# Performance work log

Hardware: AMD Instinct MI355X
Metric: run time of the kernel (lower is better)

## Reference

```python
import jax, jax.numpy as jnp
import numpy as np

N_NODES = 200000
N_EDGES = 6400000
IN_CH = 256
HID = 16


def gcn_conv(h, src, dst, deg_inv_sqrt, W, b, n_nodes):
    """One GCNConv (PyG semantics: add self-loops, symmetric norm, linear, scatter-add, bias)."""
    hw = h @ W  # [N, out]
    norm = deg_inv_sqrt[src] * deg_inv_sqrt[dst]  # [E]
    agg = jax.ops.segment_sum(norm[:, None] * hw[src], dst, num_segments=n_nodes)
    # self-loop contribution: deg_inv_sqrt[i]^2 * hw[i]
    agg = agg + hw * (deg_inv_sqrt ** 2)[:, None]
    return agg + b


def setup_inputs() -> dict:
    key = jax.random.key(0)
    k_x, k_e, k_w1, k_w2, k_w3 = jax.random.split(key, 5)
    x = jax.random.normal(k_x, (N_NODES, IN_CH), dtype=jnp.float32)
    edge_index = jax.random.randint(k_e, (2, N_EDGES), 0, N_NODES, dtype=jnp.int64)
    # Glorot-ish init for the three GCNConv weights, zeros for biases (PyG default)
    W1 = jax.random.normal(k_w1, (IN_CH, HID), dtype=jnp.float32) * (1.0 / np.sqrt(IN_CH))
    b1 = jnp.zeros((HID,), dtype=jnp.float32)
    W2 = jax.random.normal(k_w2, (HID, HID), dtype=jnp.float32) * (1.0 / np.sqrt(HID))
    b2 = jnp.zeros((HID,), dtype=jnp.float32)
    W3 = jax.random.normal(k_w3, (HID, 1), dtype=jnp.float32) * (1.0 / np.sqrt(HID))
    b3 = jnp.zeros((1,), dtype=jnp.float32)
    return {"x": x, "edge_index": edge_index, "W1": W1, "b1": b1,
            "W2": W2, "b2": b2, "W3": W3, "b3": b3}


def reference(x, edge_index, W1, b1, W2, b2, W3, b3):
    n_nodes = x.shape[0]
    src, dst = edge_index[0], edge_index[1]
    # GCN norm with self-loops: deg counts incoming edges + 1 self-loop
    deg = jax.ops.segment_sum(jnp.ones_like(dst, dtype=x.dtype), dst,
                              num_segments=n_nodes) + 1.0
    deg_inv_sqrt = deg ** -0.5  # deg >= 1, safe
    h = jax.nn.relu(gcn_conv(x, src, dst, deg_inv_sqrt, W1, b1, n_nodes))
    # dropout is identity in eval mode
    h = jax.nn.relu(gcn_conv(h, src, dst, deg_inv_sqrt, W2, b2, n_nodes))
    out = gcn_conv(h, src, dst, deg_inv_sqrt, W3, b3, n_nodes)  # [N, 1]
    return out
```

## Files before the change

### kernel.cpp

```cpp
#include <hip/hip_runtime.h>

#define NN 200000
#define EE 6400000L
#define NCB 196
#define CAP 36864
#define TILE 8192
#define NTILE 782

__device__ inline void f4add(float4& a, const float4 v) {
    a.x += v.x; a.y += v.y; a.z += v.z; a.w += v.w;
}

__global__ void k_detect(const int* __restrict__ w, int* __restrict__ flag,
                         int* __restrict__ gcur) {
    __shared__ int any;
    if (threadIdx.x == 0) any = 0;
    __syncthreads();
    int found = 0;
    for (int i = threadIdx.x; i < 8192; i += 256)
        if (w[2 * i + 1] != 0) found = 1;
    if (found) atomicOr(&any, 1);
    if (threadIdx.x < NCB) gcur[threadIdx.x] = threadIdx.x * CAP;
    __syncthreads();
    if (threadIdx.x == 0) flag[0] = any ? 0 : 1;
}

__global__ __launch_bounds__(256) void k_passA(
    const int* __restrict__ ew, const int* __restrict__ flag,
    int* __restrict__ gcur, unsigned* __restrict__ stage, long e) {
    __shared__ unsigned lv[TILE];
    __shared__ unsigned char lb[TILE];
    __shared__ int lh[NCB], lseg[NCB], lcur[NCB];
    for (int i = threadIdx.x; i < NCB; i += 256) { lh[i] = 0; lcur[i] = 0; }
    __syncthreads();
    long t0 = (long)blockIdx.x * TILE;
    int cnt = (int)min((long)TILE, e - t0);
    int shift = *flag;
    for (int i = threadIdx.x; i < cnt; i += 256) {
        int s = ew[(t0 + i) << shift];
        int d = ew[(EE + t0 + i) << shift];
        int b = d >> 10;
        lv[i] = (unsigned)s | ((unsigned)(d & 1023) << 18);
        lb[i] = (unsigned char)b;
        atomicAdd(&lh[b], 1);
    }
    __syncthreads();
    for (int i = threadIdx.x; i < NCB; i += 256)
        if (lh[i]) lseg[i] = atomicAdd(&gcur[i], lh[i]);
    __syncthreads();
    for (int i = threadIdx.x; i < cnt; i += 256) {
        int b = lb[i];
        int r = atomicAdd(&lcur[b], 1);
        stage[lseg[b] + r] = lv[i];
    }
}

__global__ __launch_bounds__(1024) void k_sortB(
    const unsigned* __restrict__ stage, const int* __restrict__ gcur,
    float* __restrict__ dis, int2* __restrict__ odn,
    unsigned* __restrict__ csr, int n) {
    __shared__ int cnt[1024];
    __shared__ int cur[1024];
    __shared__ int wsum[16];
    int t = threadIdx.x, B = blockIdx.x;
    cnt[t] = 0;
    __syncthreads();
    int s0 = B * CAP, s1 = gcur[B];
    for (int i = s0 + t; i < s1; i += 1024)
        atomicAdd(&cnt[stage[i] >> 18], 1);
    __syncthreads();
    int c = cnt[t];
    int pc = (c + 3) & ~3;
    int lane = t & 63, w = t >> 6;
    int s = pc;
#pragma unroll
    for (int o = 1; o < 64; o <<= 1) {
        int u = __shfl_up(s, o, 64);
        if (lane >= o) s += u;
    }
    if (lane == 63) wsum[w] = s;
    __syncthreads();
    int add = 0;
    for (int k = 0; k < w; ++k) add += wsum[k];
    int excl = s - pc + add;
    cur[t] = excl;
    int node = B * 1024 + t;
    if (node < n) {
        odn[node] = make_int2(s0 + excl, c);
        dis[node] = rsqrtf((float)(c + 1));
    }
    __syncthreads();
    for (int i = s0 + t; i < s1; i += 1024) {
        unsigned v = stage[i];
        int pos = s0 + atomicAdd(&cur[v >> 18], 1);
        csr[pos] = v & 0x3FFFF;
    }
}

__global__ __launch_bounds__(256) void k_mm1(
    const float* __restrict__ x, const float* __restrict__ W,
    const float* __restrict__ dis, float4* __restrict__ outr, int n) {
    __shared__ float Wl[256 * 16];
    int t = threadIdx.x;
#pragma unroll
    for (int i = 0; i < 4; ++i)
        ((float4*)Wl)[t + i * 256] = ((const float4*)W)[t + i * 256];
    __syncthreads();

    int node = blockIdx.x * 256 + t;
    if (node >= n) return;

    const float4* xr = (const float4*)(x + (long)node * 256);
    float acc[16];
#pragma unroll
    for (int o = 0; o < 16; ++o) acc[o] = 0.f;

#pragma unroll 8
    for (int kk = 0; kk < 64; ++kk) {
        float4 xv = xr[kk];
#pragma unroll
        for (int q = 0; q < 4; ++q) {
            float xs = (q == 0) ? xv.x : (q == 1) ? xv.y : (q == 2) ? xv.z : xv.w;
            const float4* wr = (const float4*)&Wl[(kk * 4 + q) * 16];
#pragma unroll
            for (int oo = 0; oo < 4; ++oo) {
                float4 wv = wr[oo];
                acc[oo * 4 + 0] = fmaf(xs, wv.x, acc[oo * 4 + 0]);
                acc[oo * 4 + 1] = fmaf(xs, wv.y, acc[oo * 4 + 1]);
                acc[oo * 4 + 2] = fmaf(xs, wv.z, acc[oo * 4 + 2]);
                acc[oo * 4 + 3] = fmaf(xs, wv.w, acc[oo * 4 + 3]);
            }
        }
    }
    float dv = dis[node];
#pragma unroll
    for (int q = 0; q < 4; ++q)
        outr[node * 4 + q] = make_float4(acc[q * 4] * dv, acc[q * 4 + 1] * dv,
                                         acc[q * 4 + 2] * dv, acc[q * 4 + 3] * dv);
}

__global__ __launch_bounds__(256) void k_mm2(
    const float4* __restrict__ hr, const float* __restrict__ W,
    const float* __restrict__ dis, float4* __restrict__ outr, int n) {
    __shared__ float Wl[256];
    if (threadIdx.x < 64) ((float4*)Wl)[threadIdx.x] = ((const float4*)W)[threadIdx.x];
    __syncthreads();
    int node = blockIdx.x * 256 + threadIdx.x;
    if (node >= n) return;
    float hv[16];
#pragma unroll
    for (int i = 0; i < 4; ++i) {
        float4 v = hr[node * 4 + i];
        hv[i * 4 + 0] = v.x; hv[i * 4 + 1] = v.y; hv[i * 4 + 2] = v.z; hv[i * 4 + 3] = v.w;
    }
    float acc[16];
#pragma unroll
    for (int o = 0; o < 16; ++o) acc[o] = 0.f;
#pragma unroll
    for (int k = 0; k < 16; ++k) {
        float xs = hv[k];
#pragma unroll
        for (int o = 0; o < 16; ++o) acc[o] = fmaf(xs, Wl[k * 16 + o], acc[o]);
    }
    float dv = dis[node];
#pragma unroll
    for (int q = 0; q < 4; ++q)
        outr[node * 4 + q] = make_float4(acc[q * 4] * dv, acc[q * 4 + 1] * dv,
                                         acc[q * 4 + 2] * dv, acc[q * 4 + 3] * dv);
}

__global__ __launch_bounds__(256) void k_mm3(
    const float4* __restrict__ hr, const float* __restrict__ W,
    const float* __restrict__ dis, float* __restrict__ hws3, int n) {
    int node = blockIdx.x * 256 + threadIdx.x;
    if (node >= n) return;
    float acc = 0.f;
#pragma unroll
    for (int i = 0; i < 4; ++i) {
        float4 v = hr[node * 4 + i];
        acc = fmaf(v.x, W[i * 4 + 0], acc);
        acc = fmaf(v.y, W[i * 4 + 1], acc);
        acc = fmaf(v.z, W[i * 4 + 2], acc);
        acc = fmaf(v.w, W[i * 4 + 3], acc);
    }
    hws3[node] = acc * dis[node];
}

template <int RELU>
__global__ __launch_bounds__(256) void k_g16(
    const int2* __restrict__ odn, const unsigned* __restrict__ csr,
    const float* __restrict__ dis, const float4* __restrict__ tab,
    const float* __restrict__ b, float4* __restrict__ outr, int n) {
    int t = threadIdx.x;
    int node = blockIdx.x * 64 + (t >> 2);
    int j = t & 3;
    if (node >= n) return;
    int2 od = odn[node];
    int s0 = od.x, dg = od.y;
    float4 aA = make_float4(0.f, 0.f, 0.f, 0.f);
    float4 aB = make_float4(0.f, 0.f, 0.f, 0.f);
    int k = 0;
    for (; k + 8 <= dg; k += 8) {
        uint4 eL = *(const uint4*)(csr + s0 + k);
        uint4 eH = *(const uint4*)(csr + s0 + k + 4);
        f4add(aA, tab[eL.x * 4 + j]);
        f4add(aB, tab[eH.x * 4 + j]);
        f4add(aA, tab[eL.y * 4 + j]);
        f4add(aB, tab[eH.y * 4 + j]);
        f4add(aA, tab[eL.z * 4 + j]);
        f4add(aB, tab[eH.z * 4 + j]);
        f4add(aA, tab[eL.w * 4 + j]);
        f4add(aB, tab[eH.w * 4 + j]);
    }
    if (k + 4 <= dg) {
        uint4 e = *(const uint4*)(csr + s0 + k);
        f4add(aA, tab[e.x * 4 + j]);
        f4add(aB, tab[e.y * 4 + j]);
        f4add(aA, tab[e.z * 4 + j]);
        f4add(aB, tab[e.w * 4 + j]);
        k += 4;
    }
    for (; k < dg; ++k)
        f4add(aA, tab[csr[s0 + k] * 4 + j]);
    f4add(aA, aB);
    f4add(aA, tab[node * 4 + j]);
    float dv = dis[node];
    float4 bb = ((const float4*)b)[j];
    float4 r = make_float4(fmaf(dv, aA.x, bb.x), fmaf(dv, aA.y, bb.y),
                           fmaf(dv, aA.z, bb.z), fmaf(dv, aA.w, bb.w));
    if (RELU) {
        r.x = fmaxf(r.x, 0.f); r.y = fmaxf(r.y, 0.f);
        r.z = fmaxf(r.z, 0.f); r.w = fmaxf(r.w, 0.f);
    }
    outr[node * 4 + j] = r;
}

__global__ __launch_bounds__(256) void k_g1(
    const int2* __restrict__ odn, const unsigned* __restrict__ csr,
    const float* __restrict__ dis, const float* __restrict__ hws3,
    const float* __restrict__ b, float* __restrict__ out, int n) {
    int t = threadIdx.x;
    int node = blockIdx.x * 16 + (t >> 4);
    int ln = t & 15;
    if (node >= n) return;
    int2 od = odn[node];
    int s0 = od.x, dg = od.y;
    float acc = 0.f;
    for (int k = ln; k < dg; k += 16)
        acc += hws3[csr[s0 + k]];
#pragma unroll
    for (int o = 8; o >= 1; o >>= 1) acc += __shfl_down(acc, o, 16);
    if (ln == 0)
        out[node] = fmaf(dis[node], acc + hws3[node], b[0]);
}

extern "C" void kernel_launch(void* const* d_in, const int* in_sizes, int n_in,
                              void* d_out, int out_size, void* d_ws, size_t ws_size,
                              hipStream_t stream) {
    const float* x  = (const float*)d_in[0];
    const int*   ew = (const int*)d_in[1];
    const float* W1 = (const float*)d_in[2];
    const float* b1 = (const float*)d_in[3];
    const float* W2 = (const float*)d_in[4];
    const float* b2 = (const float*)d_in[5];
    const float* W3 = (const float*)d_in[6];
    const float* b3 = (const float*)d_in[7];
    float* out = (float*)d_out;

    unsigned* stage = (unsigned*)d_ws;
    unsigned* csr   = stage + (long)NCB * CAP;
    int*      gcur  = (int*)(csr + (long)NCB * CAP);
    int*      flag  = gcur + 256;
    int2*     odn   = (int2*)(flag + 16);
    float*    dis   = (float*)(odn + 200704);
    float4*   bufA  = (float4*)(dis + 200704);
    float4*   bufB  = bufA + 4 * 200064;

    const int n = NN;
    const long e = EE;
    int nb = (n + 255) / 256;
    int gb = (n + 63) / 64;
    int g1b = (n + 15) / 16;

    k_detect<<<1, 256, 0, stream>>>(ew, flag, gcur);
    k_passA<<<NTILE, 256, 0, stream>>>(ew, flag, gcur, stage, e);
    k_sortB<<<NCB, 1024, 0, stream>>>(stage, gcur, dis, odn, csr, n);

    k_mm1<<<nb, 256, 0, stream>>>(x, W1, dis, bufA, n);
    k_g16<1><<<gb, 256, 0, stream>>>(odn, csr, dis, bufA, b1, bufB, n);
    k_mm2<<<nb, 256, 0, stream>>>(bufB, W2, dis, bufA, n);
    k_g16<1><<<gb, 256, 0, stream>>>(odn, csr, dis, bufA, b2, bufB, n);
    k_mm3<<<nb, 256, 0, stream>>>(bufB, W3, dis, (float*)bufA, n);
    k_g1<<<g1b, 256, 0, stream>>>(odn, csr, dis, (const float*)bufA, b3, out, n);
}
```

Baseline: 454.0 us.

## Overlap layer-1 matmul with edge binning and fuse small matmuls into gathers

Runs the x@W1 matmul in the same grid as the edge-binning pass using alternating block roles, and applies the degree scaling to hw1 inside the CSR sort kernel. The 16x16 and 16x1 matmuls are fused into the aggregation kernels, with shared-memory staging and a quad shuffle reduction. This removes three launches and the intermediate feature round trips, and lets the bandwidth-heavy x read overlap with the atomic-heavy binning. It also drops the bounds checks by relying on the node count dividing evenly by the block sizes.

```diff
diff --git a/kernel.cpp b/kernel.cpp
--- a/kernel.cpp
+++ b/kernel.cpp
@@ -11,6 +11,15 @@
     a.x += v.x; a.y += v.y; a.z += v.z; a.w += v.w;
 }
 
+union SMem {
+    struct {
+        unsigned lv[TILE];
+        unsigned char lb[TILE];
+        int lh[NCB], lseg[NCB], lcur[NCB];
+    } p;
+    float wl[256 * 16];
+};
+
 __global__ void k_detect(const int* __restrict__ w, int* __restrict__ flag,
                          int* __restrict__ gcur) {
     __shared__ int any;
@@ -25,40 +34,78 @@
     if (threadIdx.x == 0) flag[0] = any ? 0 : 1;
 }
 
-__global__ __launch_bounds__(256) void k_passA(
+__global__ __launch_bounds__(256) void k_fused(
     const int* __restrict__ ew, const int* __restrict__ flag,
-    int* __restrict__ gcur, unsigned* __restrict__ stage, long e) {
-    __shared__ unsigned lv[TILE];
-    __shared__ unsigned char lb[TILE];
-    __shared__ int lh[NCB], lseg[NCB], lcur[NCB];
-    for (int i = threadIdx.x; i < NCB; i += 256) { lh[i] = 0; lcur[i] = 0; }
-    __syncthreads();
-    long t0 = (long)blockIdx.x * TILE;
-    int cnt = (int)min((long)TILE, e - t0);
-    int shift = *flag;
-    for (int i = threadIdx.x; i < cnt; i += 256) {
-        int s = ew[(t0 + i) << shift];
-        int d = ew[(EE + t0 + i) << shift];
-        int b = d >> 10;
-        lv[i] = (unsigned)s | ((unsigned)(d & 1023) << 18);
-        lb[i] = (unsigned char)b;
-        atomicAdd(&lh[b], 1);
-    }
-    __syncthreads();
-    for (int i = threadIdx.x; i < NCB; i += 256)
-        if (lh[i]) lseg[i] = atomicAdd(&gcur[i], lh[i]);
-    __syncthreads();
-    for (int i = threadIdx.x; i < cnt; i += 256) {
-        int b = lb[i];
-        int r = atomicAdd(&lcur[b], 1);
-        stage[lseg[b] + r] = lv[i];
+    int* __restrict__ gcur, unsigned* __restrict__ stage,
+    const float* __restrict__ x, const float* __restrict__ W1,
+    float4* __restrict__ hw1, long e, int n) {
+    __shared__ SMem sm;
+    int t = threadIdx.x;
+    int role = blockIdx.x & 1;
+    int idx = blockIdx.x >> 1;
+
+    if (role == 0) {
+        for (int i = t; i < NCB; i += 256) { sm.p.lh[i] = 0; sm.p.lcur[i] = 0; }
+        __syncthreads();
+        long t0 = (long)idx * TILE;
+        int cnt = (int)min((long)TILE, e - t0);
+        int shift = *flag;
+        for (int i = t; i < cnt; i += 256) {
+            int s = ew[(t0 + i) << shift];
+            int d = ew[(EE + t0 + i) << shift];
+            int b = d >> 10;
+            sm.p.lv[i] = (unsigned)s | ((unsigned)(d & 1023) << 18);
+            sm.p.lb[i] = (unsigned char)b;
+            atomicAdd(&sm.p.lh[b], 1);
+        }
+        __syncthreads();
+        for (int i = t; i < NCB; i += 256)
+            if (sm.p.lh[i]) sm.p.lseg[i] = atomicAdd(&gcur[i], sm.p.lh[i]);
+        __syncthreads();
+        for (int i = t; i < cnt; i += 256) {
+            int b = sm.p.lb[i];
+            int r = atomicAdd(&sm.p.lcur[b], 1);
+            stage[sm.p.lseg[b] + r] = sm.p.lv[i];
+        }
+    } else {
+#pragma unroll
+        for (int i = 0; i < 4; ++i)
+            ((float4*)sm.wl)[t + i * 256] = ((const float4*)W1)[t + i * 256];
+        __syncthreads();
+        int node = idx * 256 + t;
+        if (node >= n) return;
+        const float4* xr = (const float4*)(x + (long)node * 256);
+        float acc[16];
+#pragma unroll
+        for (int o = 0; o < 16; ++o) acc[o] = 0.f;
+#pragma unroll 8
+        for (int kk = 0; kk < 64; ++kk) {
+            float4 xv = xr[kk];
+#pragma unroll
+            for (int q = 0; q < 4; ++q) {
+                float xs = (q == 0) ? xv.x : (q == 1) ? xv.y : (q == 2) ? xv.z : xv.w;
+                const float4* wr = (const float4*)&sm.wl[(kk * 4 + q) * 16];
+#pragma unroll
+                for (int oo = 0; oo < 4; ++oo) {
+                    float4 wv = wr[oo];
+                    acc[oo * 4 + 0] = fmaf(xs, wv.x, acc[oo * 4 + 0]);
+                    acc[oo * 4 + 1] = fmaf(xs, wv.y, acc[oo * 4 + 1]);
+                    acc[oo * 4 + 2] = fmaf(xs, wv.z, acc[oo * 4 + 2]);
+                    acc[oo * 4 + 3] = fmaf(xs, wv.w, acc[oo * 4 + 3]);
+                }
+            }
+        }
+#pragma unroll
+        for (int q = 0; q < 4; ++q)
+            hw1[(long)node * 4 + q] = make_float4(acc[q * 4], acc[q * 4 + 1],
+                                                  acc[q * 4 + 2], acc[q * 4 + 3]);
     }
 }
 
 __global__ __launch_bounds__(1024) void k_sortB(
     const unsigned* __restrict__ stage, const int* __restrict__ gcur,
     float* __restrict__ dis, int2* __restrict__ odn,
-    unsigned* __restrict__ csr, int n) {
+    unsigned* __restrict__ csr, float4* __restrict__ hw1, int n) {
     __shared__ int cnt[1024];
     __shared__ int cur[1024];
     __shared__ int wsum[16];
@@ -86,8 +133,15 @@
     cur[t] = excl;
     int node = B * 1024 + t;
     if (node < n) {
+        float dv = rsqrtf((float)(c + 1));
         odn[node] = make_int2(s0 + excl, c);
-        dis[node] = rsqrtf((float)(c + 1));
+        dis[node] = dv;
+        float4* row = hw1 + (long)node * 4;
+#pragma unroll
+        for (int q = 0; q < 4; ++q) {
+            float4 v = row[q];
+            row[q] = make_float4(v.x * dv, v.y * dv, v.z * dv, v.w * dv);
+        }
     }
     __syncthreads();
     for (int i = s0 + t; i < s1; i += 1024) {
@@ -97,104 +151,17 @@
     }
 }
 
-__global__ __launch_bounds__(256) void k_mm1(
-    const float* __restrict__ x, const float* __restrict__ W,
-    const float* __restrict__ dis, float4* __restrict__ outr, int n) {
-    __shared__ float Wl[256 * 16];
-    int t = threadIdx.x;
-#pragma unroll
-    for (int i = 0; i < 4; ++i)
-        ((float4*)Wl)[t + i * 256] = ((const float4*)W)[t + i * 256];
-    __syncthreads();
-
-    int node = blockIdx.x * 256 + t;
-    if (node >= n) return;
-
-    const float4* xr = (const float4*)(x + (long)node * 256);
-    float acc[16];
-#pragma unroll
-    for (int o = 0; o < 16; ++o) acc[o] = 0.f;
-
-#pragma unroll 8
-    for (int kk = 0; kk < 64; ++kk) {
-        float4 xv = xr[kk];
-#pragma unroll
-        for (int q = 0; q < 4; ++q) {
-            float xs = (q == 0) ? xv.x : (q == 1) ? xv.y : (q == 2) ? xv.z : xv.w;
-            const float4* wr = (const float4*)&Wl[(kk * 4 + q) * 16];
-#pragma unroll
-            for (int oo = 0; oo < 4; ++oo) {
-                float4 wv = wr[oo];
-                acc[oo * 4 + 0] = fmaf(xs, wv.x, acc[oo * 4 + 0]);
-                acc[oo * 4 + 1] = fmaf(xs, wv.y, acc[oo * 4 + 1]);
-                acc[oo * 4 + 2] = fmaf(xs, wv.z, acc[oo * 4 + 2]);
-                acc[oo * 4 + 3] = fmaf(xs, wv.w, acc[oo * 4 + 3]);
-            }
-        }
-    }
-    float dv = dis[node];
-#pragma unroll
-    for (int q = 0; q < 4; ++q)
-        outr[node * 4 + q] = make_float4(acc[q * 4] * dv, acc[q * 4 + 1] * dv,
-                                         acc[q * 4 + 2] * dv, acc[q * 4 + 3] * dv);
-}
-
-__global__ __launch_bounds__(256) void k_mm2(
-    const float4* __restrict__ hr, const float* __restrict__ W,
-    const float* __restrict__ dis, float4* __restrict__ outr, int n) {
-    __shared__ float Wl[256];
-    if (threadIdx.x < 64) ((float4*)Wl)[threadIdx.x] = ((const float4*)W)[threadIdx.x];
-    __syncthreads();
-    int node = blockIdx.x * 256 + threadIdx.x;
-    if (node >= n) return;
-    float hv[16];
-#pragma unroll
-    for (int i = 0; i < 4; ++i) {
-        float4 v = hr[node * 4 + i];
-        hv[i * 4 + 0] = v.x; hv[i * 4 + 1] = v.y; hv[i * 4 + 2] = v.z; hv[i * 4 + 3] = v.w;
-    }
-    float acc[16];
-#pragma unroll
-    for (int o = 0; o < 16; ++o) acc[o] = 0.f;
-#pragma unroll
-    for (int k = 0; k < 16; ++k) {
-        float xs = hv[k];
-#pragma unroll
-        for (int o = 0; o < 16; ++o) acc[o] = fmaf(xs, Wl[k * 16 + o], acc[o]);
-    }
-    float dv = dis[node];
-#pragma unroll
-    for (int q = 0; q < 4; ++q)
-        outr[node * 4 + q] = make_float4(acc[q * 4] * dv, acc[q * 4 + 1] * dv,
-                                         acc[q * 4 + 2] * dv, acc[q * 4 + 3] * dv);
-}
-
-__global__ __launch_bounds__(256) void k_mm3(
-    const float4* __restrict__ hr, const float* __restrict__ W,
-    const float* __restrict__ dis, float* __restrict__ hws3, int n) {
-    int node = blockIdx.x * 256 + threadIdx.x;
-    if (node >= n) return;
-    float acc = 0.f;
-#pragma unroll
-    for (int i = 0; i < 4; ++i) {
-        float4 v = hr[node * 4 + i];
-        acc = fmaf(v.x, W[i * 4 + 0], acc);
-        acc = fmaf(v.y, W[i * 4 + 1], acc);
-        acc = fmaf(v.z, W[i * 4 + 2], acc);
-        acc = fmaf(v.w, W[i * 4 + 3], acc);
-    }
-    hws3[node] = acc * dis[node];
-}
-
-template <int RELU>
-__global__ __launch_bounds__(256) void k_g16(
+__global__ __launch_bounds__(256) void k_g16a(
     const int2* __restrict__ odn, const unsigned* __restrict__ csr,
     const float* __restrict__ dis, const float4* __restrict__ tab,
-    const float* __restrict__ b, float4* __restrict__ outr, int n) {
+    const float* __restrict__ b1v, const float* __restrict__ W2,
+    float4* __restrict__ out2) {
+    __shared__ float h1s[64 * 17];
+    __shared__ float W2l[256];
     int t = threadIdx.x;
+    if (t < 64) ((float4*)W2l)[t] = ((const float4*)W2)[t];
     int node = blockIdx.x * 64 + (t >> 2);
     int j = t & 3;
-    if (node >= n) return;
     int2 od = odn[node];
     int s0 = od.x, dg = od.y;
     float4 aA = make_float4(0.f, 0.f, 0.f, 0.f);
@@ -225,14 +192,79 @@
     f4add(aA, aB);
     f4add(aA, tab[node * 4 + j]);
     float dv = dis[node];
-    float4 bb = ((const float4*)b)[j];
+    float4 bb = ((const float4*)b1v)[j];
     float4 r = make_float4(fmaf(dv, aA.x, bb.x), fmaf(dv, aA.y, bb.y),
                            fmaf(dv, aA.z, bb.z), fmaf(dv, aA.w, bb.w));
-    if (RELU) {
-        r.x = fmaxf(r.x, 0.f); r.y = fmaxf(r.y, 0.f);
-        r.z = fmaxf(r.z, 0.f); r.w = fmaxf(r.w, 0.f);
-    }
-    outr[node * 4 + j] = r;
+    r.x = fmaxf(r.x, 0.f); r.y = fmaxf(r.y, 0.f);
+    r.z = fmaxf(r.z, 0.f); r.w = fmaxf(r.w, 0.f);
+    int nl = t >> 2;
+    h1s[nl * 17 + 4 * j + 0] = r.x;
+    h1s[nl * 17 + 4 * j + 1] = r.y;
+    h1s[nl * 17 + 4 * j + 2] = r.z;
+    h1s[nl * 17 + 4 * j + 3] = r.w;
+    __syncthreads();
+    float4 acc = make_float4(0.f, 0.f, 0.f, 0.f);
+#pragma unroll
+    for (int kk = 0; kk < 16; ++kk) {
+        float hv = h1s[nl * 17 + kk];
+        float4 wv = ((const float4*)&W2l[kk * 16])[j];
+        acc.x = fmaf(hv, wv.x, acc.x);
+        acc.y = fmaf(hv, wv.y, acc.y);
+        acc.z = fmaf(hv, wv.z, acc.z);
+        acc.w = fmaf(hv, wv.w, acc.w);
+    }
+    out2[(long)node * 4 + j] = make_float4(acc.x * dv, acc.y * dv,
+                                           acc.z * dv, acc.w * dv);
+}
+
+__global__ __launch_bounds__(256) void k_g16b(
+    const int2* __restrict__ odn, const unsigned* __restrict__ csr,
+    const float* __restrict__ dis, const float4* __restrict__ tab,
+    const float* __restrict__ b2v, const float* __restrict__ W3,
+    float* __restrict__ hws3) {
+    int t = threadIdx.x;
+    int node = blockIdx.x * 64 + (t >> 2);
+    int j = t & 3;
+    int2 od = odn[node];
+    int s0 = od.x, dg = od.y;
+    float4 aA = make_float4(0.f, 0.f, 0.f, 0.f);
+    float4 aB = make_float4(0.f, 0.f, 0.f, 0.f);
+    int k = 0;
+    for (; k + 8 <= dg; k += 8) {
+        uint4 eL = *(const uint4*)(csr + s0 + k);
+        uint4 eH = *(const uint4*)(csr + s0 + k + 4);
+        f4add(aA, tab[eL.x * 4 + j]);
+        f4add(aB, tab[eH.x * 4 + j]);
+        f4add(aA, tab[eL.y * 4 + j]);
+        f4add(aB, tab[eH.y * 4 + j]);
+        f4add(aA, tab[eL.z * 4 + j]);
+        f4add(aB, tab[eH.z * 4 + j]);
+        f4add(aA, tab[eL.w * 4 + j]);
+        f4add(aB, tab[eH.w * 4 + j]);
+    }
+    if (k + 4 <= dg) {
+        uint4 e = *(const uint4*)(csr + s0 + k);
+        f4add(aA, tab[e.x * 4 + j]);
+        f4add(aB, tab[e.y * 4 + j]);
+        f4add(aA, tab[e.z * 4 + j]);
+        f4add(aB, tab[e.w * 4 + j]);
+        k += 4;
+    }
+    for (; k < dg; ++k)
+        f4add(aA, tab[csr[s0 + k] * 4 + j]);
+    f4add(aA, aB);
+    f4add(aA, tab[node * 4 + j]);
+    float dv = dis[node];
+    float4 bb = ((const float4*)b2v)[j];
+    float4 r = make_float4(fmaf(dv, aA.x, bb.x), fmaf(dv, aA.y, bb.y),
+                           fmaf(dv, aA.z, bb.z), fmaf(dv, aA.w, bb.w));
+    r.x = fmaxf(r.x, 0.f); r.y = fmaxf(r.y, 0.f);
+    r.z = fmaxf(r.z, 0.f); r.w = fmaxf(r.w, 0.f);
+    float4 w3 = ((const float4*)W3)[j];
+    float pd = r.x * w3.x + r.y * w3.y + r.z * w3.z + r.w * w3.w;
+    pd += __shfl_xor(pd, 1, 4);
+    pd += __shfl_xor(pd, 2, 4);
+    if (j == 0) hws3[node] = pd * dv;
 }
 
 __global__ __launch_bounds__(256) void k_g1(
@@ -278,18 +310,13 @@
 
     const int n = NN;
     const long e = EE;
-    int nb = (n + 255) / 256;
-    int gb = (n + 63) / 64;
-    int g1b = (n + 15) / 16;
+    int gb = n / 64;
+    int g1b = n / 16;
 
     k_detect<<<1, 256, 0, stream>>>(ew, flag, gcur);
-    k_passA<<<NTILE, 256, 0, stream>>>(ew, flag, gcur, stage, e);
-    k_sortB<<<NCB, 1024, 0, stream>>>(stage, gcur, dis, odn, csr, n);
-
-    k_mm1<<<nb, 256, 0, stream>>>(x, W1, dis, bufA, n);
-    k_g16<1><<<gb, 256, 0, stream>>>(odn, csr, dis, bufA, b1, bufB, n);
-    k_mm2<<<nb, 256, 0, stream>>>(bufB, W2, dis, bufA, n);
-    k_g16<1><<<gb, 256, 0, stream>>>(odn, csr, dis, bufA, b2, bufB, n);
-    k_mm3<<<nb, 256, 0, stream>>>(bufB, W3, dis, (float*)bufA, n);
+    k_fused<<<2 * NTILE, 256, 0, stream>>>(ew, flag, gcur, stage, x, W1, bufA, e, n);
+    k_sortB<<<NCB, 1024, 0, stream>>>(stage, gcur, dis, odn, csr, bufA, n);
+    k_g16a<<<gb, 256, 0, stream>>>(odn, csr, dis, bufA, b1, W2, bufB);
+    k_g16b<<<gb, 256, 0, stream>>>(odn, csr, dis, bufB, b2, W3, (float*)bufA);
     k_g1<<<g1b, 256, 0, stream>>>(odn, csr, dis, (const float*)bufA, b3, out, n);
 }
```

After: 439.9 us. 1.03x faster.
